# Kernel optimization log

Measured on AMD Instinct MI355X. Metric: run time of the kernel, lower is better.

The kernel has to match this reference:

```python
import math
import jax, jax.numpy as jnp
import numpy as np

B, S = 2, 2048
D, H, DK = 1024, 16, 64
M = 16            # nb_features
L = 4             # n_layers
DFF = 4096
VS, VT = 69, 69   # src/tgt vocab
NU = 10000        # num_users
FD = 34           # feature_dim
EPS = 1e-6


def make_pe(seq_len, d_model):
    pos = np.arange(seq_len, dtype=np.float32)[:, None]
    div = np.exp(np.arange(0, d_model, 2, dtype=np.float32) * (-math.log(10000.0) / d_model))
    pe = np.zeros((seq_len, d_model), np.float32)
    pe[:, 0::2] = np.sin(pos * div)
    pe[:, 1::2] = np.cos(pos * div)
    return jnp.asarray(pe)


def gelu_approx(x):
    return 0.5 * x * (1.0 + jnp.tanh(math.sqrt(2.0 / math.pi) * (x + 0.044715 * x ** 3)))


def layer_norm(x, alpha, bias):
    # torch LayerNormalization: unbiased std, eps added to std
    mu = x.mean(-1, keepdims=True)
    var = ((x - mu) ** 2).sum(-1, keepdims=True) / (x.shape[-1] - 1)
    return alpha * (x - mu) / (jnp.sqrt(var) + EPS) + bias


def setup_inputs():
    key = jax.random.key(0)
    ks = jax.random.split(key, 24)
    w = lambda k, shape, s=0.02: (jax.random.normal(k, shape, jnp.float32) * s)
    inp = {}
    inp['ids'] = jax.random.randint(ks[0], (B, S), 0, VS)
    inp['user_ids'] = jax.random.randint(ks[1], (B,), 0, NU)
    inp['id_embed'] = w(ks[2], (VS, D), 1.0)
    inp['feat_proj'] = w(ks[3], (D, FD))
    inp['gamma'] = jnp.float32(1.0)
    inp['gate_logits'] = w(ks[4], (NU, H))
    inp['wq'] = w(ks[5], (L, D, D))
    inp['wk'] = w(ks[6], (L, D, D))
    inp['wv'] = w(ks[7], (L, D, D))
    inp['wo'] = w(ks[8], (L, D, D))
    inp['omega'] = jax.random.normal(ks[9], (L, M, DK), jnp.float32) / math.sqrt(DK)
    inp['ln1_a'] = jnp.ones((L, D)); inp['ln1_b'] = jnp.zeros((L, D))
    inp['ln2_a'] = jnp.ones((L, D)); inp['ln2_b'] = jnp.zeros((L, D))
    inp['ff_w1'] = w(ks[10], (L, DFF, D)); inp['ff_b1'] = jnp.zeros((L, DFF))
    inp['ff_w2'] = w(ks[11], (L, D, DFF)); inp['ff_b2'] = jnp.zeros((L, D))
    inp['fin_a'] = jnp.ones((D,)); inp['fin_b'] = jnp.zeros((D,))
    inp['proj_w'] = w(ks[12], (VT, D)); inp['proj_b'] = jnp.zeros((VT,))
    inp['feat_tbl'] = w(ks[13], (VS, FD), 1.0)
    pm = np.zeros(VS, bool); pm[10:] = True   # ids >= 10 are products
    inp['prod_mask'] = jnp.asarray(pm)
    inp['pe'] = make_pe(S, D)
    return inp


def performer(xn, wq, wk, wv, wo, omega, gate):
    b, sq, _ = xn.shape
    q = (xn @ wq.T).reshape(b, sq, H, DK)
    k = (xn @ wk.T).reshape(b, sq, H, DK)
    v = (xn @ wv.T).reshape(b, sq, H, DK)
    # exp kernel feature map + row normalization
    qp = jnp.exp(-0.5 * (q @ omega.T) ** 2)        # (B,S,H,M)
    kp = jnp.exp(-0.5 * (k @ omega.T) ** 2)
    qp = qp / (qp.sum(-1, keepdims=True) + EPS)
    kp = kp / (kp.sum(-1, keepdims=True) + EPS)
    K_cum = jnp.cumsum(kp, axis=1)                              # (B,S,H,M)
    KV_cum = jnp.cumsum(kp[..., None] * v[..., None, :], axis=1)  # (B,S,H,M,DK)
    # blockwise causal index (block_size_h = block_size_w = 1)
    bh, bw = 1, 1
    ki = jnp.minimum((jnp.arange(sq) // bh + 1) * bw - 1, sq - 1)
    Ks = jnp.take(K_cum, ki, axis=1)
    KVs = jnp.take(KV_cum, ki, axis=1)
    num = jnp.einsum('bshm,bshmd->bshd', qp, KVs)
    den = jnp.sum(qp * Ks, -1, keepdims=True)
    out = num / (den + EPS)
    out = out * gate[:, None, :, None]
    return out.reshape(b, sq, D) @ wo.T


def reference(ids, user_ids, id_embed, feat_proj, gamma, gate_logits,
              wq, wk, wv, wo, omega, ln1_a, ln1_b, ln2_a, ln2_b,
              ff_w1, ff_b1, ff_w2, ff_b2, fin_a, fin_b,
              proj_w, proj_b, feat_tbl, prod_mask, pe):
    # SpecialPlusFeatureLookup
    id_vec = id_embed[ids]                       # (B,S,D)
    feat_vec = feat_tbl[ids] @ feat_proj.T       # (B,S,D)
    keep = prod_mask[ids]
    x = id_vec + gamma * (feat_vec * keep[..., None])
    # positional encoding (dropout=eval -> identity)
    x = x + pe[None, :x.shape[1], :]
    # per-user head gate
    gate = jax.nn.softmax(gate_logits[user_ids], axis=-1)  # (B,H)
    for l in range(L):
        x = x + performer(layer_norm(x, ln1_a[l], ln1_b[l]),
                          wq[l], wk[l], wv[l], wo[l], omega[l], gate)
        xn = layer_norm(x, ln2_a[l], ln2_b[l])
        x = x + (gelu_approx(xn @ ff_w1[l].T + ff_b1[l]) @ ff_w2[l].T + ff_b2[l])
    x = layer_norm(x, fin_a, fin_b)
    return x @ proj_w.T + proj_b                 # (B,S,VT)
```

## Files before the change

kernel.cpp:

```cpp
#include <hip/hip_runtime.h>
#include <hip/hip_bf16.h>
#include <math.h>

constexpr int BB  = 2;
constexpr int SS  = 2048;
constexpr int DD  = 1024;
constexpr int HH  = 16;
constexpr int DKK = 64;
constexpr int MB  = 16;
constexpr int LL  = 4;
constexpr int DF  = 4096;
constexpr int VSZ = 69;
constexpr int VTT = 69;
constexpr int FDD = 34;
constexpr float EPSF = 1e-6f;
constexpr int CL = 32;
constexpr int NC = SS / CL;

typedef unsigned short u16;
typedef unsigned int   u32;
using bf16x8 = __attribute__((ext_vector_type(8))) short;
using f32x4  = __attribute__((ext_vector_type(4))) float;

static __device__ __forceinline__ float b2f(u16 u) {
    union { u32 i; float f; } p; p.i = ((u32)u) << 16; return p.f;
}
static __device__ __forceinline__ u16 f2b(float f) {
    union { float f; u32 i; } p; p.f = f;
    u32 r = p.i + 0x7fffu + ((p.i >> 16) & 1u);
    return (u16)(r >> 16);
}
static __device__ __forceinline__ u32 pack2(float lo, float hi) {
    __hip_bfloat162 h = __float22bfloat162_rn(make_float2(lo, hi));
    return *(u32*)&h;
}
static __device__ __forceinline__ float gelu_f(float x) {
    float z = 0.7978845608028654f * (x + 0.044715f * x * x * x);
    z = fminf(fmaxf(z, -10.f), 10.f);
    float e = __expf(2.f * z);
    float th = (e - 1.f) / (e + 1.f);
    return 0.5f * x * (1.f + th);
}
static __device__ __forceinline__ float ldg1(const void* p, size_t i, int f32) {
    return f32 ? ((const float*)p)[i] : b2f(((const u16*)p)[i]);
}
static __device__ __forceinline__ float4 ldg4(const void* p, size_t i, int f32) {
    if (f32) return *(const float4*)((const float*)p + i);
    ushort4 u = *(const ushort4*)((const u16*)p + i);
    return make_float4(b2f(u.x), b2f(u.y), b2f(u.z), b2f(u.w));
}

#define GLD16(gp, lp) __builtin_amdgcn_global_load_lds( \
    (const __attribute__((address_space(1))) void*)(gp), \
    (__attribute__((address_space(3))) void*)(lp), 16, 0, 0)

__global__ void k_flag(const void* __restrict__ gamma, int* __restrict__ flag) {
    if (threadIdx.x == 0) *flag = (((const u16*)gamma)[0] == 0) ? 1 : 0;
}

__global__ __launch_bounds__(256) void k_build_tbl(
    const void* __restrict__ id_embed, const void* __restrict__ feat_tbl,
    const void* __restrict__ feat_proj, const void* __restrict__ gamma,
    const int* __restrict__ flagp, float* __restrict__ tbl)
{
    const int f32 = *flagp;
    int idx = blockIdx.x * 256 + threadIdx.x;
    if (idx >= VSZ * DD) return;
    int id = idx / DD, d = idx % DD;
    float acc = ldg1(id_embed, idx, f32);
    if (id >= 10) {
        float g = ldg1(gamma, 0, f32);
        float s = 0.f;
        for (int f = 0; f < FDD; ++f)
            s += ldg1(feat_tbl, (size_t)id * FDD + f, f32) * ldg1(feat_proj, (size_t)d * FDD + f, f32);
        acc += g * s;
    }
    tbl[idx] = acc;
}

__global__ __launch_bounds__(256) void k_gather(
    const float* __restrict__ tbl, const int* __restrict__ ids,
    const void* __restrict__ pe, const int* __restrict__ flagp, float* __restrict__ x)
{
    const int f32 = *flagp;
    int idx = blockIdx.x * 256 + threadIdx.x;
    int bs = idx >> 10, d = idx & (DD - 1);
    int s = bs & (SS - 1);
    x[idx] = tbl[ids[bs] * DD + d] + ldg1(pe, (size_t)s * DD + d, f32);
}

__global__ void k_gate(const void* __restrict__ gl, const int* __restrict__ uid,
                       const int* __restrict__ flagp, float* __restrict__ gate)
{
    const int f32 = *flagp;
    int b = threadIdx.x;
    if (b >= BB) return;
    size_t off = (size_t)uid[b] * HH;
    float v[HH], mx = -1e30f;
    for (int i = 0; i < HH; ++i) { v[i] = ldg1(gl, off + i, f32); mx = fmaxf(mx, v[i]); }
    float s = 0.f;
    for (int i = 0; i < HH; ++i) { v[i] = expf(v[i] - mx); s += v[i]; }
    for (int i = 0; i < HH; ++i) gate[b * HH + i] = v[i] / s;
}

__global__ __launch_bounds__(256) void k_layernorm(
    const float* __restrict__ x, const void* __restrict__ alpha,
    const void* __restrict__ beta, size_t p_off,
    const int* __restrict__ flagp, u16* __restrict__ y)
{
    const int f32 = *flagp;
    int row = blockIdx.x;
    const float* xr = x + (size_t)row * DD;
    int t = threadIdx.x;
    float v[4]; float s = 0.f;
    #pragma unroll
    for (int j = 0; j < 4; ++j) { v[j] = xr[t + j * 256]; s += v[j]; }
    __shared__ float red[8];
    int lane = t & 63, wv = t >> 6;
    #pragma unroll
    for (int off = 32; off > 0; off >>= 1) s += __shfl_down(s, off, 64);
    if (lane == 0) red[wv] = s;
    __syncthreads();
    float mu = (red[0] + red[1] + red[2] + red[3]) * (1.f / DD);
    __syncthreads();
    float ss = 0.f;
    #pragma unroll
    for (int j = 0; j < 4; ++j) { float dv = v[j] - mu; ss += dv * dv; }
    #pragma unroll
    for (int off = 32; off > 0; off >>= 1) ss += __shfl_down(ss, off, 64);
    if (lane == 0) red[wv] = ss;
    __syncthreads();
    float var = (red[0] + red[1] + red[2] + red[3]) * (1.f / (DD - 1));
    float rs = 1.f / (sqrtf(var) + EPSF);
    u16* yr = y + (size_t)row * DD;
    #pragma unroll
    for (int j = 0; j < 4; ++j) {
        int d = t + j * 256;
        yr[d] = f2b(ldg1(alpha, p_off + d, f32) * (v[j] - mu) * rs + ldg1(beta, p_off + d, f32));
    }
}

template<int BM>
static __device__ __forceinline__ void gemm_core(
    const u16* __restrict__ A, const void* __restrict__ W, size_t w_off, int ldw,
    const void* __restrict__ bias, size_t b_off, int f32,
    int K, int O, int act, int mode, u16* __restrict__ Cb, float* __restrict__ resid,
    int bx, int by)
{
    constexpr int NJ = (BM == 128) ? 4 : 2;
    __shared__ u16 As[BM * 32];
    __shared__ u16 Bs[128 * 32];
    int t = threadIdx.x;
    int lane = t & 63, w = t >> 6;
    int quad = lane >> 4, l16 = lane & 15;
    int wm = (BM == 128) ? (w >> 1) * 64 : 0;
    int wn = (BM == 128) ? (w & 1) * 64 : w * 32;
    int n0 = by * BM, o0 = bx * 128;

    f32x4 acc[4][NJ];
    #pragma unroll
    for (int i = 0; i < 4; ++i)
        #pragma unroll
        for (int j = 0; j < NJ; ++j)
            #pragma unroll
            for (int r = 0; r < 4; ++r) acc[i][j][r] = 0.f;

    int r0 = t >> 2, c0 = (t & 3) * 8;
    const u16* Ap = A + (size_t)n0 * K + c0;
    char* AsB = (char*)As;
    char* BsB = (char*)Bs;

    for (int k0 = 0; k0 < K; k0 += 32) {
        GLD16(Ap + (size_t)r0 * K + k0, AsB + t * 16);
        if (BM == 128)
            GLD16(Ap + (size_t)(r0 + 64) * K + k0, AsB + 4096 + t * 16);
        if (f32) {
            const float* Wf = (const float*)W + w_off + k0 + c0;
            const float* p0 = Wf + (size_t)(o0 + r0) * ldw;
            const float* p1 = p0 + (size_t)64 * ldw;
            float4 xa = *(const float4*)p0, xb = *(const float4*)(p0 + 4);
            uint4 pk;
            pk.x = pack2(xa.x, xa.y); pk.y = pack2(xa.z, xa.w);
            pk.z = pack2(xb.x, xb.y); pk.w = pack2(xb.z, xb.w);
            *(uint4*)(BsB + t * 16) = pk;
            float4 ya = *(const float4*)p1, yb = *(const float4*)(p1 + 4);
            pk.x = pack2(ya.x, ya.y); pk.y = pack2(ya.z, ya.w);
            pk.z = pack2(yb.x, yb.y); pk.w = pack2(yb.z, yb.w);
            *(uint4*)(BsB + 4096 + t * 16) = pk;
        } else {
            const u16* Wb = (const u16*)W + w_off + k0 + c0;
            GLD16(Wb + (size_t)(o0 + r0) * ldw, BsB + t * 16);
            GLD16(Wb + (size_t)(o0 + r0 + 64) * ldw, BsB + 4096 + t * 16);
        }
        __syncthreads();
        bf16x8 af[4], bfv[NJ];
        #pragma unroll
        for (int i = 0; i < 4; ++i)
            af[i] = *(const bf16x8*)(As + (size_t)(wm + i * 16 + l16) * 32 + quad * 8);
        #pragma unroll
        for (int j = 0; j < NJ; ++j)
            bfv[j] = *(const bf16x8*)(Bs + (size_t)(wn + j * 16 + l16) * 32 + quad * 8);
        #pragma unroll
        for (int i = 0; i < 4; ++i)
            #pragma unroll
            for (int j = 0; j < NJ; ++j)
                acc[i][j] = __builtin_amdgcn_mfma_f32_16x16x32_bf16(af[i], bfv[j], acc[i][j], 0, 0, 0);
        __syncthreads();
    }
    #pragma unroll
    for (int i = 0; i < 4; ++i) {
        #pragma unroll
        for (int j = 0; j < NJ; ++j) {
            int col = o0 + wn + j * 16 + l16;
            float bval = bias ? ldg1(bias, b_off + col, f32) : 0.f;
            #pragma unroll
            for (int r = 0; r < 4; ++r) {
                int row = n0 + wm + i * 16 + quad * 4 + r;
                float val = acc[i][j][r] + bval;
                if (act) val = gelu_f(val);
                size_t idx = (size_t)row * O + col;
                if (mode == 1) resid[idx] += val;
                else           Cb[idx] = f2b(val);
            }
        }
    }
}

__global__ __launch_bounds__(256) void k_gemm128(
    const u16* __restrict__ A, const void* __restrict__ W, size_t w_off, int ldw,
    const void* __restrict__ bias, size_t b_off, const int* __restrict__ flagp,
    int K, int O, int act, int mode, u16* __restrict__ Cb, float* __restrict__ resid)
{
    gemm_core<128>(A, W, w_off, ldw, bias, b_off, *flagp, K, O, act, mode, Cb, resid,
                   blockIdx.x, blockIdx.y);
}

__global__ __launch_bounds__(256) void k_gemm64(
    const u16* __restrict__ A, const void* __restrict__ W, size_t w_off, int ldw,
    const void* __restrict__ bias, size_t b_off, const int* __restrict__ flagp,
    int K, int O, int act, int mode, u16* __restrict__ Cb, float* __restrict__ resid)
{
    gemm_core<64>(A, W, w_off, ldw, bias, b_off, *flagp, K, O, act, mode, Cb, resid,
                  blockIdx.x, blockIdx.y);
}

__global__ __launch_bounds__(256) void k_gemm_qkv(
    const u16* __restrict__ A,
    const void* __restrict__ Wq, const void* __restrict__ Wk, const void* __restrict__ Wv,
    size_t w_off, const int* __restrict__ flagp,
    u16* __restrict__ oq, u16* __restrict__ ok, u16* __restrict__ ov)
{
    const void* W = (blockIdx.z == 0) ? Wq : (blockIdx.z == 1) ? Wk : Wv;
    u16* o = (blockIdx.z == 0) ? oq : (blockIdx.z == 1) ? ok : ov;
    gemm_core<128>(A, W, w_off, DD, nullptr, 0, *flagp, DD, DD, 0, 0, o, nullptr,
                   blockIdx.x, blockIdx.y);
}

__global__ __launch_bounds__(256) void k_gemm_small(
    const u16* __restrict__ A, const void* __restrict__ W, size_t w_off, int ldw,
    const void* __restrict__ bias, size_t b_off,
    const int* __restrict__ flagp, int K, int O, void* __restrict__ outp)
{
    const int f32 = *flagp;
    __shared__ float As[16][68];
    __shared__ float Ws[16][68];
    int t = threadIdx.x;
    int tx = t & 15, ty = t >> 4;
    int o0 = blockIdx.x * 64, n0 = blockIdx.y * 64;
    int lr = t >> 2;
    int lk = (t & 3) * 4;
    float c[4][4] = {};
    for (int k0 = 0; k0 < K; k0 += 16) {
        ushort4 av = *(const ushort4*)(A + (size_t)(n0 + lr) * K + k0 + lk);
        As[lk + 0][lr] = b2f(av.x); As[lk + 1][lr] = b2f(av.y);
        As[lk + 2][lr] = b2f(av.z); As[lk + 3][lr] = b2f(av.w);
        float4 wv4 = make_float4(0.f, 0.f, 0.f, 0.f);
        int orow = o0 + lr;
        if (orow < O) wv4 = ldg4(W, w_off + (size_t)orow * ldw + k0 + lk, f32);
        Ws[lk + 0][lr] = wv4.x; Ws[lk + 1][lr] = wv4.y;
        Ws[lk + 2][lr] = wv4.z; Ws[lk + 3][lr] = wv4.w;
        __syncthreads();
        #pragma unroll
        for (int kk = 0; kk < 16; ++kk) {
            float4 a = *(const float4*)&As[kk][ty * 4];
            float4 b = *(const float4*)&Ws[kk][tx * 4];
            c[0][0] += a.x * b.x; c[0][1] += a.x * b.y; c[0][2] += a.x * b.z; c[0][3] += a.x * b.w;
            c[1][0] += a.y * b.x; c[1][1] += a.y * b.y; c[1][2] += a.y * b.z; c[1][3] += a.y * b.w;
            c[2][0] += a.z * b.x; c[2][1] += a.z * b.y; c[2][2] += a.z * b.z; c[2][3] += a.z * b.w;
            c[3][0] += a.w * b.x; c[3][1] += a.w * b.y; c[3][2] += a.w * b.z; c[3][3] += a.w * b.w;
        }
        __syncthreads();
    }
    #pragma unroll
    for (int i = 0; i < 4; ++i) {
        int n = n0 + ty * 4 + i;
        #pragma unroll
        for (int j = 0; j < 4; ++j) {
            int o = o0 + tx * 4 + j;
            if (o >= O) continue;
            float val = c[i][j];
            if (bias) val += ldg1(bias, b_off + o, f32);
            size_t idx = (size_t)n * O + o;
            if (f32) ((float*)outp)[idx] = val;
            else     ((u16*)outp)[idx] = f2b(val);
        }
    }
}

__global__ __launch_bounds__(256) void k_featmap(
    const u16* __restrict__ q, const void* __restrict__ omega, size_t o_off,
    const int* __restrict__ flagp, u16* __restrict__ qp_t)
{
    const int f32 = *flagp;
    __shared__ float q_s[64][68];
    __shared__ float om_s[16][68];
    int t = threadIdx.x;
    int bh = blockIdx.y, b = bh >> 4, h = bh & 15;
    int s0 = blockIdx.x * 64;
    const u16* qbase = q + (size_t)(b * SS + s0) * DD + h * DKK;
    #pragma unroll
    for (int i = 0; i < 2; ++i) {
        int idx = i * 256 + t;
        int si = idx >> 3, part = idx & 7;
        uint4 raw = *(const uint4*)(qbase + (size_t)si * DD + part * 8);
        const u16* pr = (const u16*)&raw;
        *(float4*)&q_s[si][part * 8]     = make_float4(b2f(pr[0]), b2f(pr[1]), b2f(pr[2]), b2f(pr[3]));
        *(float4*)&q_s[si][part * 8 + 4] = make_float4(b2f(pr[4]), b2f(pr[5]), b2f(pr[6]), b2f(pr[7]));
    }
    #pragma unroll
    for (int i = 0; i < 4; ++i) {
        int idx = i * 256 + t;
        om_s[idx >> 6][idx & 63] = ldg1(omega, o_off + idx, f32);
    }
    __syncthreads();
    int s = t >> 2, mg = t & 3;
    float u[4] = {0.f, 0.f, 0.f, 0.f};
    #pragma unroll
    for (int dk = 0; dk < 64; dk += 4) {
        float4 q4 = *(const float4*)&q_s[s][dk];
        #pragma unroll
        for (int mj = 0; mj < 4; ++mj) {
            float4 o4 = *(const float4*)&om_s[mg * 4 + mj][dk];
            u[mj] += q4.x * o4.x + q4.y * o4.y + q4.z * o4.z + q4.w * o4.w;
        }
    }
    float phi[4], tot = 0.f;
    #pragma unroll
    for (int mj = 0; mj < 4; ++mj) { phi[mj] = expf(-0.5f * u[mj] * u[mj]); tot += phi[mj]; }
    tot += __shfl_xor(tot, 1); tot += __shfl_xor(tot, 2);
    float inv = 1.f / (tot + EPSF);
    uint2 out;
    out.x = pack2(phi[0] * inv, phi[1] * inv);
    out.y = pack2(phi[2] * inv, phi[3] * inv);
    *(uint2*)(qp_t + ((size_t)bh * SS + s0 + s) * MB + mg * 4) = out;
}

__global__ __launch_bounds__(64) void k_scan_part(
    const u16* __restrict__ kp_t, const u16* __restrict__ v,
    float* __restrict__ kv_tot, float* __restrict__ kc_tot)
{
    int c = blockIdx.x, bh = blockIdx.y;
    int b = bh >> 4, h = bh & 15;
    int d = threadIdx.x;
    __shared__ float kp_s[CL * MB];
    const u16* kpb = kp_t + ((size_t)bh * SS + c * CL) * MB;
    #pragma unroll
    for (int i = 0; i < CL * MB / 64; ++i) {
        int idx = i * 64 + d;
        kp_s[idx] = b2f(kpb[idx]);
    }
    __syncthreads();
    float Kc[MB], KV[MB];
    #pragma unroll
    for (int m = 0; m < MB; ++m) { Kc[m] = 0.f; KV[m] = 0.f; }
    const u16* vp = v + ((size_t)b * SS + c * CL) * DD + h * DKK + d;
    for (int si = 0; si < CL; ++si) {
        float vd = b2f(vp[(size_t)si * DD]);
        #pragma unroll
        for (int m = 0; m < MB; ++m) {
            float kp = kp_s[si * MB + m];
            Kc[m] += kp; KV[m] += kp * vd;
        }
    }
    float* kvp = kv_tot + (((size_t)bh * NC + c) * MB) * DKK + d;
    #pragma unroll
    for (int m = 0; m < MB; ++m) kvp[(size_t)m * DKK] = KV[m];
    #pragma unroll
    for (int m = 0; m < MB; ++m)
        if (d == m) kc_tot[((size_t)bh * NC + c) * MB + m] = Kc[m];
}

__global__ __launch_bounds__(64) void k_scan_off(
    float* __restrict__ kv_tot, float* __restrict__ kc_tot)
{
    int bh = blockIdx.x; int d = threadIdx.x;
    if (d < MB) {
        float run = 0.f;
        for (int c = 0; c < NC; ++c) {
            size_t i = ((size_t)bh * NC + c) * MB + d;
            float tt = kc_tot[i]; kc_tot[i] = run; run += tt;
        }
    }
    float run[MB];
    #pragma unroll
    for (int m = 0; m < MB; ++m) run[m] = 0.f;
    for (int c = 0; c < NC; ++c) {
        size_t base = (((size_t)bh * NC + c) * MB) * DKK + d;
        float tt[MB];
        #pragma unroll
        for (int m = 0; m < MB; ++m) tt[m] = kv_tot[base + (size_t)m * DKK];
        #pragma unroll
        for (int m = 0; m < MB; ++m) { kv_tot[base + (size_t)m * DKK] = run[m]; run[m] += tt[m]; }
    }
}

__global__ __launch_bounds__(64) void k_scan_out(
    const u16* __restrict__ qp_t, const u16* __restrict__ kp_t, const u16* __restrict__ v,
    const float* __restrict__ kv_tot, const float* __restrict__ kc_tot,
    const float* __restrict__ gate, u16* __restrict__ attn)
{
    int c = blockIdx.x, bh = blockIdx.y;
    int b = bh >> 4, h = bh & 15;
    int d = threadIdx.x;
    __shared__ float kp_s[CL * MB], qp_s[CL * MB];
    const u16* kpb = kp_t + ((size_t)bh * SS + c * CL) * MB;
    const u16* qpb = qp_t + ((size_t)bh * SS + c * CL) * MB;
    #pragma unroll
    for (int i = 0; i < CL * MB / 64; ++i) {
        int idx = i * 64 + d;
        kp_s[idx] = b2f(kpb[idx]);
        qp_s[idx] = b2f(qpb[idx]);
    }
    __syncthreads();
    float Kc[MB], KV[MB];
    const float* kvp = kv_tot + (((size_t)bh * NC + c) * MB) * DKK + d;
    const float* kcp = kc_tot + ((size_t)bh * NC + c) * MB;
    #pragma unroll
    for (int m = 0; m < MB; ++m) { KV[m] = kvp[(size_t)m * DKK]; Kc[m] = kcp[m]; }
    float g = gate[bh];
    const u16* vp = v + ((size_t)b * SS + c * CL) * DD + h * DKK + d;
    u16* ap = attn + ((size_t)b * SS + c * CL) * DD + h * DKK + d;
    for (int si = 0; si < CL; ++si) {
        float vd = b2f(vp[(size_t)si * DD]);
        float num = 0.f, den = 0.f;
        #pragma unroll
        for (int m = 0; m < MB; ++m) {
            float kp = kp_s[si * MB + m];
            Kc[m] += kp; KV[m] += kp * vd;
            float qp = qp_s[si * MB + m];
            num += qp * KV[m]; den += qp * Kc[m];
        }
        ap[(size_t)si * DD] = f2b(num / (den + EPSF) * g);
    }
}

extern "C" void kernel_launch(void* const* d_in, const int* in_sizes, int n_in,
                              void* d_out, int out_size, void* d_ws, size_t ws_size,
                              hipStream_t stream)
{
    const int*  ids       = (const int*)d_in[0];
    const int*  user_ids  = (const int*)d_in[1];
    const void* id_embed  = d_in[2];
    const void* feat_proj = d_in[3];
    const void* gamma     = d_in[4];
    const void* gate_log  = d_in[5];
    const void* wq        = d_in[6];
    const void* wk        = d_in[7];
    const void* wv        = d_in[8];
    const void* wo        = d_in[9];
    const void* omega     = d_in[10];
    const void* ln1_a     = d_in[11];
    const void* ln1_b     = d_in[12];
    const void* ln2_a     = d_in[13];
    const void* ln2_b     = d_in[14];
    const void* ff_w1     = d_in[15];
    const void* ff_b1     = d_in[16];
    const void* ff_w2     = d_in[17];
    const void* ff_b2     = d_in[18];
    const void* fin_a     = d_in[19];
    const void* fin_b     = d_in[20];
    const void* proj_w    = d_in[21];
    const void* proj_b    = d_in[22];
    const void* feat_tbl  = d_in[23];
    const void* pe        = d_in[25];

    char* base = (char*)d_ws;
    const size_t MiB = (size_t)1 << 20;
    int*   flagp  = (int*)base;
    float* gate   = (float*)(base + 64);
    float* kc_tot = (float*)(base + 4096);
    float* tbl    = (float*)(base + 256 * 1024);
    float* x      = (float*)(base + 1 * MiB);
    u16*   xn     = (u16*)  (base + 17 * MiB);
    float* kv_tot = (float*)(base + 17 * MiB);
    u16*   qb     = (u16*)  (base + 25 * MiB);
    u16*   kb     = (u16*)  (base + 33 * MiB);
    u16*   vb     = (u16*)  (base + 41 * MiB);
    u16*   qp_t   = (u16*)  (base + 49 * MiB);
    u16*   kp_t   = (u16*)  (base + 51 * MiB);
    u16*   attn   = qb;
    u16*   ff1c   = qb;

    const int NT = BB * SS;

    k_flag<<<1, 64, 0, stream>>>(gamma, flagp);
    k_build_tbl<<<(VSZ * DD + 255) / 256, 256, 0, stream>>>(id_embed, feat_tbl, feat_proj, gamma, flagp, tbl);
    k_gather<<<(NT * DD) / 256, 256, 0, stream>>>(tbl, ids, pe, flagp, x);
    k_gate<<<1, 64, 0, stream>>>(gate_log, user_ids, flagp, gate);

    dim3 gQKV(DD / 128, NT / 128, 3);
    dim3 gWo(DD / 128, NT / 64);
    dim3 gF1(2048 / 128, NT / 128);
    dim3 gF2(DD / 128, NT / 64);
    dim3 gFeat(SS / 64, BB * HH);
    dim3 gScan(NC, BB * HH);

    for (int l = 0; l < LL; ++l) {
        size_t lDD = (size_t)l * DD * DD;
        k_layernorm<<<NT, 256, 0, stream>>>(x, ln1_a, ln1_b, (size_t)l * DD, flagp, xn);
        k_gemm_qkv<<<gQKV, 256, 0, stream>>>(xn, wq, wk, wv, lDD, flagp, qb, kb, vb);
        k_featmap<<<gFeat, 256, 0, stream>>>(qb, omega, (size_t)l * MB * DKK, flagp, qp_t);
        k_featmap<<<gFeat, 256, 0, stream>>>(kb, omega, (size_t)l * MB * DKK, flagp, kp_t);
        k_scan_part<<<gScan, 64, 0, stream>>>(kp_t, vb, kv_tot, kc_tot);
        k_scan_off<<<BB * HH, 64, 0, stream>>>(kv_tot, kc_tot);
        k_scan_out<<<gScan, 64, 0, stream>>>(qp_t, kp_t, vb, kv_tot, kc_tot, gate, attn);
        k_gemm64<<<gWo, 256, 0, stream>>>(attn, wo, lDD, DD, nullptr, 0, flagp, DD, DD, 0, 1, nullptr, x);
        k_layernorm<<<NT, 256, 0, stream>>>(x, ln2_a, ln2_b, (size_t)l * DD, flagp, xn);
        for (int c = 0; c < 2; ++c) {
            size_t w1_off = (size_t)l * DF * DD + (size_t)c * 2048 * DD;
            size_t b1_off = (size_t)l * DF + c * 2048;
            size_t w2_off = (size_t)l * DD * DF + (size_t)c * 2048;
            k_gemm128<<<gF1, 256, 0, stream>>>(xn, ff_w1, w1_off, DD, ff_b1, b1_off, flagp, DD, 2048, 1, 0, ff1c, nullptr);
            k_gemm64<<<gF2, 256, 0, stream>>>(ff1c, ff_w2, w2_off, DF,
                                              (c == 0) ? ff_b2 : nullptr, (size_t)l * DD,
                                              flagp, 2048, DD, 0, 1, nullptr, x);
        }
    }
    k_layernorm<<<NT, 256, 0, stream>>>(x, fin_a, fin_b, 0, flagp, xn);
    dim3 g4((VTT + 63) / 64, NT / 64);
    k_gemm_small<<<g4, 256, 0, stream>>>(xn, proj_w, 0, DD, proj_b, 0, flagp, DD, VTT, d_out);
}
```

Baseline: 2.008 ms.

## Double-buffer GEMM shared-memory tiles to overlap global loads with MFMA

The shared GEMM core now keeps two A/B tiles in LDS. It issues the next K-slice's global loads (and, for fp32 weights, register prefetch plus convert-and-store) while computing on the current tile, so the loop needs one barrier per iteration instead of two. This aims to hide global memory latency behind the matrix-core work in all the dense projections. It doubles LDS use per block and raises register pressure, which may reduce occupancy. An explicit lda parameter is also threaded through the kernels, with the same values as before.

```diff
diff --git a/kernel.cpp b/kernel.cpp
--- a/kernel.cpp
+++ b/kernel.cpp
@@ -142,14 +142,15 @@
 
 template<int BM>
 static __device__ __forceinline__ void gemm_core(
-    const u16* __restrict__ A, const void* __restrict__ W, size_t w_off, int ldw,
+    const u16* __restrict__ A, int lda,
+    const void* __restrict__ W, size_t w_off, int ldw,
     const void* __restrict__ bias, size_t b_off, int f32,
     int K, int O, int act, int mode, u16* __restrict__ Cb, float* __restrict__ resid,
     int bx, int by)
 {
     constexpr int NJ = (BM == 128) ? 4 : 2;
-    __shared__ u16 As[BM * 32];
-    __shared__ u16 Bs[128 * 32];
+    __shared__ u16 As[2][BM * 32];
+    __shared__ u16 Bs[2][128 * 32];
     int t = threadIdx.x;
     int lane = t & 63, w = t >> 6;
     int quad = lane >> 4, l16 = lane & 15;
@@ -166,47 +167,71 @@
             for (int r = 0; r < 4; ++r) acc[i][j][r] = 0.f;
 
     int r0 = t >> 2, c0 = (t & 3) * 8;
-    const u16* Ap = A + (size_t)n0 * K + c0;
-    char* AsB = (char*)As;
-    char* BsB = (char*)Bs;
-
-    for (int k0 = 0; k0 < K; k0 += 32) {
-        GLD16(Ap + (size_t)r0 * K + k0, AsB + t * 16);
+    const u16* Ap = A + (size_t)n0 * lda + c0;
+    float4 wr[4];
+
+    auto stageA = [&](int buf, int k0) {
+        GLD16(Ap + (size_t)r0 * lda + k0, (char*)As[buf] + t * 16);
         if (BM == 128)
-            GLD16(Ap + (size_t)(r0 + 64) * K + k0, AsB + 4096 + t * 16);
-        if (f32) {
-            const float* Wf = (const float*)W + w_off + k0 + c0;
-            const float* p0 = Wf + (size_t)(o0 + r0) * ldw;
-            const float* p1 = p0 + (size_t)64 * ldw;
-            float4 xa = *(const float4*)p0, xb = *(const float4*)(p0 + 4);
-            uint4 pk;
-            pk.x = pack2(xa.x, xa.y); pk.y = pack2(xa.z, xa.w);
-            pk.z = pack2(xb.x, xb.y); pk.w = pack2(xb.z, xb.w);
-            *(uint4*)(BsB + t * 16) = pk;
-            float4 ya = *(const float4*)p1, yb = *(const float4*)(p1 + 4);
-            pk.x = pack2(ya.x, ya.y); pk.y = pack2(ya.z, ya.w);
-            pk.z = pack2(yb.x, yb.y); pk.w = pack2(yb.z, yb.w);
-            *(uint4*)(BsB + 4096 + t * 16) = pk;
-        } else {
-            const u16* Wb = (const u16*)W + w_off + k0 + c0;
-            GLD16(Wb + (size_t)(o0 + r0) * ldw, BsB + t * 16);
-            GLD16(Wb + (size_t)(o0 + r0 + 64) * ldw, BsB + 4096 + t * 16);
-        }
-        __syncthreads();
+            GLD16(Ap + (size_t)(r0 + 64) * lda + k0, (char*)As[buf] + 4096 + t * 16);
+    };
+    auto stageBbf = [&](int buf, int k0) {
+        const u16* Wb = (const u16*)W + w_off + k0 + c0;
+        GLD16(Wb + (size_t)(o0 + r0) * ldw, (char*)Bs[buf] + t * 16);
+        GLD16(Wb + (size_t)(o0 + r0 + 64) * ldw, (char*)Bs[buf] + 4096 + t * 16);
+    };
+    auto loadWf = [&](int k0) {
+        const float* Wf = (const float*)W + w_off + k0 + c0;
+        const float* p0 = Wf + (size_t)(o0 + r0) * ldw;
+        const float* p1 = p0 + (size_t)64 * ldw;
+        wr[0] = *(const float4*)p0; wr[1] = *(const float4*)(p0 + 4);
+        wr[2] = *(const float4*)p1; wr[3] = *(const float4*)(p1 + 4);
+    };
+    auto writeWf = [&](int buf) {
+        uint4 pk;
+        pk.x = pack2(wr[0].x, wr[0].y); pk.y = pack2(wr[0].z, wr[0].w);
+        pk.z = pack2(wr[1].x, wr[1].y); pk.w = pack2(wr[1].z, wr[1].w);
+        *(uint4*)((char*)Bs[buf] + t * 16) = pk;
+        pk.x = pack2(wr[2].x, wr[2].y); pk.y = pack2(wr[2].z, wr[2].w);
+        pk.z = pack2(wr[3].x, wr[3].y); pk.w = pack2(wr[3].z, wr[3].w);
+        *(uint4*)((char*)Bs[buf] + 4096 + t * 16) = pk;
+    };
+    auto compute = [&](int buf) {
         bf16x8 af[4], bfv[NJ];
         #pragma unroll
         for (int i = 0; i < 4; ++i)
-            af[i] = *(const bf16x8*)(As + (size_t)(wm + i * 16 + l16) * 32 + quad * 8);
+            af[i] = *(const bf16x8*)(As[buf] + (size_t)(wm + i * 16 + l16) * 32 + quad * 8);
         #pragma unroll
         for (int j = 0; j < NJ; ++j)
-            bfv[j] = *(const bf16x8*)(Bs + (size_t)(wn + j * 16 + l16) * 32 + quad * 8);
+            bfv[j] = *(const bf16x8*)(Bs[buf] + (size_t)(wn + j * 16 + l16) * 32 + quad * 8);
         #pragma unroll
         for (int i = 0; i < 4; ++i)
             #pragma unroll
             for (int j = 0; j < NJ; ++j)
                 acc[i][j] = __builtin_amdgcn_mfma_f32_16x16x32_bf16(af[i], bfv[j], acc[i][j], 0, 0, 0);
+    };
+
+    if (f32) { loadWf(0); stageA(0, 0); writeWf(0); }
+    else     { stageA(0, 0); stageBbf(0, 0); }
+    __syncthreads();
+
+    int cur = 0;
+    for (int k0 = 32; k0 < K; k0 += 32) {
+        if (f32) {
+            loadWf(k0);
+            stageA(cur ^ 1, k0);
+            compute(cur);
+            writeWf(cur ^ 1);
+        } else {
+            stageA(cur ^ 1, k0);
+            stageBbf(cur ^ 1, k0);
+            compute(cur);
+        }
         __syncthreads();
-    }
+        cur ^= 1;
+    }
+    compute(cur);
+
     #pragma unroll
     for (int i = 0; i < 4; ++i) {
         #pragma unroll
@@ -227,20 +252,20 @@
 }
 
 __global__ __launch_bounds__(256) void k_gemm128(
-    const u16* __restrict__ A, const void* __restrict__ W, size_t w_off, int ldw,
+    const u16* __restrict__ A, int lda, const void* __restrict__ W, size_t w_off, int ldw,
     const void* __restrict__ bias, size_t b_off, const int* __restrict__ flagp,
     int K, int O, int act, int mode, u16* __restrict__ Cb, float* __restrict__ resid)
 {
-    gemm_core<128>(A, W, w_off, ldw, bias, b_off, *flagp, K, O, act, mode, Cb, resid,
+    gemm_core<128>(A, lda, W, w_off, ldw, bias, b_off, *flagp, K, O, act, mode, Cb, resid,
                    blockIdx.x, blockIdx.y);
 }
 
 __global__ __launch_bounds__(256) void k_gemm64(
-    const u16* __restrict__ A, const void* __restrict__ W, size_t w_off, int ldw,
+    const u16* __restrict__ A, int lda, const void* __restrict__ W, size_t w_off, int ldw,
     const void* __restrict__ bias, size_t b_off, const int* __restrict__ flagp,
     int K, int O, int act, int mode, u16* __restrict__ Cb, float* __restrict__ resid)
 {
-    gemm_core<64>(A, W, w_off, ldw, bias, b_off, *flagp, K, O, act, mode, Cb, resid,
+    gemm_core<64>(A, lda, W, w_off, ldw, bias, b_off, *flagp, K, O, act, mode, Cb, resid,
                   blockIdx.x, blockIdx.y);
 }
 
@@ -252,7 +277,7 @@
 {
     const void* W = (blockIdx.z == 0) ? Wq : (blockIdx.z == 1) ? Wk : Wv;
     u16* o = (blockIdx.z == 0) ? oq : (blockIdx.z == 1) ? ok : ov;
-    gemm_core<128>(A, W, w_off, DD, nullptr, 0, *flagp, DD, DD, 0, 0, o, nullptr,
+    gemm_core<128>(A, DD, W, w_off, DD, nullptr, 0, *flagp, DD, DD, 0, 0, o, nullptr,
                    blockIdx.x, blockIdx.y);
 }
 
@@ -524,14 +549,14 @@
         k_scan_part<<<gScan, 64, 0, stream>>>(kp_t, vb, kv_tot, kc_tot);
         k_scan_off<<<BB * HH, 64, 0, stream>>>(kv_tot, kc_tot);
         k_scan_out<<<gScan, 64, 0, stream>>>(qp_t, kp_t, vb, kv_tot, kc_tot, gate, attn);
-        k_gemm64<<<gWo, 256, 0, stream>>>(attn, wo, lDD, DD, nullptr, 0, flagp, DD, DD, 0, 1, nullptr, x);
+        k_gemm64<<<gWo, 256, 0, stream>>>(attn, DD, wo, lDD, DD, nullptr, 0, flagp, DD, DD, 0, 1, nullptr, x);
         k_layernorm<<<NT, 256, 0, stream>>>(x, ln2_a, ln2_b, (size_t)l * DD, flagp, xn);
         for (int c = 0; c < 2; ++c) {
             size_t w1_off = (size_t)l * DF * DD + (size_t)c * 2048 * DD;
             size_t b1_off = (size_t)l * DF + c * 2048;
             size_t w2_off = (size_t)l * DD * DF + (size_t)c * 2048;
-            k_gemm128<<<gF1, 256, 0, stream>>>(xn, ff_w1, w1_off, DD, ff_b1, b1_off, flagp, DD, 2048, 1, 0, ff1c, nullptr);
-            k_gemm64<<<gF2, 256, 0, stream>>>(ff1c, ff_w2, w2_off, DF,
+            k_gemm128<<<gF1, 256, 0, stream>>>(xn, DD, ff_w1, w1_off, DD, ff_b1, b1_off, flagp, DD, 2048, 1, 0, ff1c, nullptr);
+            k_gemm64<<<gF2, 256, 0, stream>>>(ff1c, 2048, ff_w2, w2_off, DF,
                                               (c == 0) ? ff_b2 : nullptr, (size_t)l * DD,
                                               flagp, 2048, DD, 0, 1, nullptr, x);
         }
```

New measurement: 2.222 ms. 1.11x slower.
